# Kernel optimization log

Hardware: AMD Instinct MI355X
Metric: run time of the kernel (lower is better)

Reference implementation:

```python
import jax, jax.numpy as jnp
import numpy as np

DIN = 256
N_RATIOS = 3          # cfg.ANCHOR_RATIOS = [0.5, 1, 2]
NC_SCORE = N_RATIOS * 2   # 6
NC_BBOX = N_RATIOS * 4    # 12
LEVEL_SHAPES = [(150, 250), (75, 125), (38, 63), (19, 32), (10, 16)]


def setup_inputs() -> dict:
    key = jax.random.key(0)
    ks = jax.random.split(key, 12)
    inp = {}
    for i, (h, w) in enumerate(LEVEL_SHAPES):
        inp[f"rpn_feat_p{i+2}"] = jax.random.normal(ks[i], (4, DIN, h, w), dtype=jnp.float32)
    inp["im_info"] = jnp.ones((4, 3), dtype=jnp.float32)
    s = 0.01
    inp["W_conv"] = jax.random.normal(ks[5], (512, DIN, 3, 3), dtype=jnp.float32) * s
    inp["b_conv"] = jnp.zeros((512,), dtype=jnp.float32)
    inp["W_cls"] = jax.random.normal(ks[6], (NC_SCORE, 512), dtype=jnp.float32) * s
    inp["b_cls"] = jnp.zeros((NC_SCORE,), dtype=jnp.float32)
    inp["W_box"] = jax.random.normal(ks[7], (NC_BBOX, 512), dtype=jnp.float32) * s
    inp["b_box"] = jnp.zeros((NC_BBOX,), dtype=jnp.float32)
    return inp


def _conv3x3(x, W, b):
    y = jax.lax.conv_general_dilated(
        x, W, window_strides=(1, 1), padding="SAME",
        dimension_numbers=("NCHW", "OIHW", "NCHW"))
    return y + b[None, :, None, None]


def _level_head(feat, W_conv, b_conv, W_cls, b_cls, W_box, b_box):
    B = feat.shape[0]
    conv1 = jax.nn.relu(_conv3x3(feat, W_conv, b_conv))            # [B,512,H,W]
    score = jnp.einsum("bchw,oc->bohw", conv1, W_cls) + b_cls[None, :, None, None]  # [B,6,H,W]
    bbox = jnp.einsum("bchw,oc->bohw", conv1, W_box) + b_box[None, :, None, None]   # [B,12,H,W]
    _, C, H, W = score.shape
    # reshape(x, 2): view(B, 2, C*H/2, W), softmax over dim 1, reshape back
    prob = jax.nn.softmax(score.reshape(B, 2, (C * H) // 2, W), axis=1).reshape(B, C, H, W)
    score_f = score.transpose(0, 2, 3, 1).reshape(B, -1, 2)
    prob_f = prob.transpose(0, 2, 3, 1).reshape(B, -1, 2)
    bbox_f = bbox.transpose(0, 2, 3, 1).reshape(B, -1, 4)
    return score_f, prob_f, bbox_f


def reference(rpn_feat_p2, rpn_feat_p3, rpn_feat_p4, rpn_feat_p5, rpn_feat_p6,
              im_info, W_conv, b_conv, W_cls, b_cls, W_box, b_box):
    feats = [rpn_feat_p2, rpn_feat_p3, rpn_feat_p4, rpn_feat_p5, rpn_feat_p6]
    scores, probs, boxes = [], [], []
    for f in feats:  # fixed 5 FPN levels
        s, p, b = _level_head(f, W_conv, b_conv, W_cls, b_cls, W_box, b_box)
        scores.append(s); probs.append(p); boxes.append(b)
    rpn_cls_score_alls = jnp.concatenate(scores, axis=1)            # [B, N, 2]
    rpn_cls_prob_alls = jnp.concatenate(probs, axis=1)              # [B, N, 2]
    rpn_bbox_pred_alls = jnp.concatenate(boxes, axis=1)             # [B, N, 4]
    return rpn_cls_score_alls, rpn_cls_prob_alls, rpn_bbox_pred_alls
```

## Files before the change

### kernel.cpp

```cpp
#include <hip/hip_runtime.h>
#include <stdint.h>


typedef __bf16 bf16x8 __attribute__((ext_vector_type(8)));
typedef float  f32x4  __attribute__((ext_vector_type(4)));

#define WS_WR2_OFF   0
#define WS_WH2_OFF   2359296
#define WS_SB_OFF    2392064
#define WS_FP_OFF    17100800
#define WS_TOTAL     123197440

__device__ __forceinline__ unsigned short f2bf(float f) {
    unsigned u = __builtin_bit_cast(unsigned, f);
    unsigned r = (u + 0x7FFF + ((u >> 16) & 1)) >> 16;
    return (unsigned short)r;
}

__device__ __forceinline__ void gl_lds16(const void* g, void* l) {
    __builtin_amdgcn_global_load_lds(
        (const __attribute__((address_space(1))) unsigned int*)g,
        (__attribute__((address_space(3))) unsigned int*)l, 16, 0, 0);
}

__global__ __launch_bounds__(256) void prep_weights(
    const float* __restrict__ Wc, const float* __restrict__ Wcls,
    const float* __restrict__ Wbox,
    unsigned short* __restrict__ wr2, unsigned short* __restrict__ wh2)
{
    int idx = blockIdx.x * 256 + threadIdx.x;
    if (idx < 1179648) {
        int o = idx / 2304;
        int k = idx - o * 2304;
        int r = k >> 8, c = k & 255;
        wr2[idx] = f2bf(Wc[o * 2304 + c * 9 + r]);
    } else {
        int i2 = idx - 1179648;
        if (i2 < 9216) {
            int j = i2 >> 9, o = i2 & 511;
            float v = (j < 6) ? Wcls[j * 512 + o] : Wbox[(j - 6) * 512 + o];
            wh2[j * 512 + o] = f2bf(v);
        }
    }
}

__global__ __launch_bounds__(256) void prep_feats(
    const float* __restrict__ f0, const float* __restrict__ f1,
    const float* __restrict__ f2, const float* __restrict__ f3,
    const float* __restrict__ f4, unsigned short* __restrict__ fpad)
{
    __shared__ unsigned short lds[64 * 258];
    int bi = blockIdx.x;
    int b = bi / 817;
    int r = bi - b * 817;
    const float* fsrc; int H, W, Wp, h, wb; long lb;
    if (r < 600)      { fsrc=f0; H=150; W=250; Wp=252; h=r>>2; wb=r&3; lb=32768    + (long)b*9805824; }
    else if (r < 750) { int rr=r-600; fsrc=f1; H=75; W=125; Wp=127; h=rr>>1; wb=rr&1; lb=39288832 + (long)b*2503424; }
    else if (r < 788) { fsrc=f2; H=38; W=63; Wp=65; h=r-750; wb=0; lb=49335296 + (long)b*665600; }
    else if (r < 807) { fsrc=f3; H=19; W=32; Wp=34; h=r-788; wb=0; lb=52030464 + (long)b*182784; }
    else              { fsrc=f4; H=10; W=16; Wp=18; h=r-807; wb=0; lb=52794368 + (long)b*55296; }
    const int t = threadIdx.x;
    const long cstr = (long)H * W;
    const int w = t & 63;
    const int wg = wb * 64 + w;
    const bool wv = (wg < W);
    const float* src = fsrc + (((long)b * 256) * H + h) * W + wg;
    unsigned* ldsw = (unsigned*)lds;
    #pragma unroll 4
    for (int it = 0; it < 32; ++it) {
        int c0 = (t >> 6) * 2 + it * 8;
        float v0 = wv ? src[(long)c0 * cstr] : 0.0f;
        float v1 = wv ? src[(long)(c0 + 1) * cstr] : 0.0f;
        unsigned pk = (unsigned)f2bf(v0) | ((unsigned)f2bf(v1) << 16);
        ldsw[w * 129 + (c0 >> 1)] = pk;
    }
    __syncthreads();
    #pragma unroll
    for (int k = 0; k < 8; ++k) {
        int g  = k * 256 + t;
        int px = g >> 5;
        int pg = wb * 64 + px;
        if (pg >= W) continue;
        int d0 = px * 129 + (g & 31) * 4;
        uint4 v;
        v.x = ldsw[d0]; v.y = ldsw[d0 + 1]; v.z = ldsw[d0 + 2]; v.w = ldsw[d0 + 3];
        unsigned short* dst = fpad + lb + (long)((h + 1) * Wp + (pg + 1)) * 256 + (g & 31) * 8;
        *(uint4*)dst = v;
    }
}

__global__ __launch_bounds__(256) void conv_main(
    const unsigned short* __restrict__ fpad,
    const unsigned short* __restrict__ wr2,
    const unsigned short* __restrict__ wh2,
    const float* __restrict__ b_conv,
    float* __restrict__ sbuf)
{
    __shared__ unsigned short smem[16384];
    const int tid = threadIdx.x;
    const int bx = blockIdx.x;
    const int tile = bx >> 2, chunk = bx & 3;
    int b = tile / 399;
    int tr = tile - b * 399;
    int Wp, lt; long lb;
    if (tr < 296)      { lt = tr;       Wp = 252; lb = 32768    + (long)b * 9805824; }
    else if (tr < 371) { lt = tr - 296; Wp = 127; lb = 39288832 + (long)b * 2503424; }
    else if (tr < 391) { lt = tr - 371; Wp = 65;  lb = 49335296 + (long)b * 665600;  }
    else if (tr < 397) { lt = tr - 391; Wp = 34;  lb = 52030464 + (long)b * 182784;  }
    else               { lt = tr - 397; Wp = 18;  lb = 52794368 + (long)b * 55296;   }

    const int arow  = tid >> 3;
    const int aslot = (tid & 7) ^ (arow & 7);
    const long apix = lb + (long)(Wp + lt * 128 + arow) * 256 + aslot * 8;
    const long bofs = (long)(chunk * 128 + arow) * 2304 + aslot * 8;

    const int wv = tid >> 6, lane = tid & 63;
    char* lA = (char*)smem + wv * 1024;
    char* lB = (char*)smem + 16384 + wv * 1024;
    const int mrow = (wv & 1) * 64, ncol = (wv >> 1) * 64;
    const int mr = lane & 15;
    const int kq = (lane >> 4) * 8;
    const int m7 = mr & 7;

    f32x4 acc[4][4];
    #pragma unroll
    for (int mt = 0; mt < 4; ++mt)
        #pragma unroll
        for (int nt = 0; nt < 4; ++nt) acc[mt][nt] = (f32x4){0.f, 0.f, 0.f, 0.f};

    for (int r = 0; r < 9; ++r) {
        const int doff = (r / 3 - 1) * Wp + (r % 3 - 1);
        const unsigned short* ga = fpad + apix + (long)doff * 256;
        const unsigned short* gb = wr2 + bofs + r * 256;
        for (int cb = 0; cb < 4; ++cb) {
            const unsigned short* ga2 = ga + cb * 64;
            const unsigned short* gb2 = gb + cb * 64;
            #pragma unroll
            for (int i = 0; i < 4; ++i) {
                gl_lds16(ga2 + i * 8192,  lA + i * 4096);
                gl_lds16(gb2 + i * 73728, lB + i * 4096);
            }
            __syncthreads();
            #pragma unroll
            for (int kk = 0; kk < 64; kk += 32) {
                const int sx = ((((kk >> 3) + (lane >> 4)) ^ m7) << 3);
                bf16x8 af[4], bfr[4];
                #pragma unroll
                for (int mt = 0; mt < 4; ++mt)
                    af[mt] = *(const bf16x8*)&smem[(mrow + mt * 16 + mr) * 64 + sx];
                #pragma unroll
                for (int nt = 0; nt < 4; ++nt)
                    bfr[nt] = *(const bf16x8*)&smem[8192 + (ncol + nt * 16 + mr) * 64 + sx];
                #pragma unroll
                for (int mt = 0; mt < 4; ++mt)
                    #pragma unroll
                    for (int nt = 0; nt < 4; ++nt)
                        acc[mt][nt] = __builtin_amdgcn_mfma_f32_16x16x32_bf16(
                            af[mt], bfr[nt], acc[mt][nt], 0, 0, 0);
            }
            __syncthreads();
        }
    }

    float bias[4];
    #pragma unroll
    for (int nt = 0; nt < 4; ++nt) bias[nt] = b_conv[chunk * 128 + ncol + nt * 16 + mr];
    #pragma unroll
    for (int mt = 0; mt < 4; ++mt)
        #pragma unroll
        for (int nt = 0; nt < 4; ++nt)
            #pragma unroll
            for (int q = 0; q < 4; ++q) {
                int row = mrow + mt * 16 + (lane >> 4) * 4 + q;
                int col = ncol + nt * 16 + mr;
                int sl  = (col >> 3) ^ (row & 7);
                smem[row * 128 + (sl << 3) + (col & 7)] =
                    f2bf(fmaxf(acc[mt][nt][q] + bias[nt], 0.0f));
            }
    __syncthreads();

    f32x4 acc2[2][2];
    #pragma unroll
    for (int mi = 0; mi < 2; ++mi)
        #pragma unroll
        for (int ni = 0; ni < 2; ++ni) acc2[mi][ni] = (f32x4){0.f, 0.f, 0.f, 0.f};
    #pragma unroll
    for (int ks = 0; ks < 4; ++ks) {
        const int sg = ks * 4 + (lane >> 4);
        bf16x8 ha[2], hb[2];
        #pragma unroll
        for (int mi = 0; mi < 2; ++mi) {
            int rowH = (wv * 2 + mi) * 16 + mr;
            ha[mi] = *(const bf16x8*)&smem[rowH * 128 + ((sg ^ m7) << 3)];
        }
        #pragma unroll
        for (int ni = 0; ni < 2; ++ni)
            hb[ni] = *(const bf16x8*)&wh2[(ni * 16 + mr) * 512 + chunk * 128 + ks * 32 + kq];
        #pragma unroll
        for (int mi = 0; mi < 2; ++mi)
            #pragma unroll
            for (int ni = 0; ni < 2; ++ni)
                acc2[mi][ni] = __builtin_amdgcn_mfma_f32_16x16x32_bf16(
                    ha[mi], hb[ni], acc2[mi][ni], 0, 0, 0);
    }
    const long slotbase = (long)tile * 128;
    #pragma unroll
    for (int ni = 0; ni < 2; ++ni) {
        int j = ni * 16 + mr;
        if (j < 18) {
            #pragma unroll
            for (int mi = 0; mi < 2; ++mi)
                #pragma unroll
                for (int q = 0; q < 4; ++q) {
                    int row = (wv * 2 + mi) * 16 + (lane >> 4) * 4 + q;
                    atomicAdd(&sbuf[(slotbase + row) * 18 + j], acc2[mi][ni][q]);
                }
        }
    }
}

__global__ __launch_bounds__(256) void finalize(
    const float* __restrict__ sbuf, const float* __restrict__ b_cls,
    const float* __restrict__ b_box, float* __restrict__ out)
{
    int idx = blockIdx.x * 256 + threadIdx.x;
    int tile = idx >> 7, m = idx & 127;
    int b = tile / 399;
    int tr = tile - b * 399;
    int hp, wp, H, W, noff;
    if (tr < 296)      { int f = 252 + (tr)       * 128 + m; hp = f / 252; wp = f - hp * 252; H = 150; W = 250; noff = 0; }
    else if (tr < 371) { int f = 127 + (tr - 296) * 128 + m; hp = f / 127; wp = f - hp * 127; H = 75;  W = 125; noff = 112500; }
    else if (tr < 391) { int f = 65  + (tr - 371) * 128 + m; hp = f / 65;  wp = f - hp * 65;  H = 38;  W = 63;  noff = 140625; }
    else if (tr < 397) { int f = 34  + (tr - 391) * 128 + m; hp = f / 34;  wp = f - hp * 34;  H = 19;  W = 32;  noff = 147807; }
    else               { int f = 18  + (tr - 397) * 128 + m; hp = f / 18;  wp = f - hp * 18;  H = 10;  W = 16;  noff = 149631; }
    if (hp < 1 || hp > H || wp < 1 || wp > W) return;

    const float* s = sbuf + (long)idx * 18;
    float sc[6], bb[12], pr[6];
    #pragma unroll
    for (int c = 0; c < 6; ++c) sc[c] = s[c] + b_cls[c];
    #pragma unroll
    for (int k = 0; k < 12; ++k) bb[k] = s[6 + k] + b_box[k];
    #pragma unroll
    for (int c = 0; c < 6; ++c) {
        int p = (c < 3) ? c + 3 : c - 3;
        pr[c] = 1.0f / (1.0f + expf(sc[p] - sc[c]));
    }
    int n = noff + ((hp - 1) * W + (wp - 1)) * 3;
    long o0 = ((long)b * 150111 + n) * 2;
    float* O0 = out + o0;
    float* O1 = out + 1200888 + o0;
    float* O2 = out + 2401776 + ((long)b * 150111 + n) * 4;
    #pragma unroll
    for (int c = 0; c < 6; ++c) { O0[c] = sc[c]; O1[c] = pr[c]; }
    #pragma unroll
    for (int k = 0; k < 12; ++k) O2[k] = bb[k];
}

extern "C" void kernel_launch(void* const* d_in, const int* in_sizes, int n_in,
                              void* d_out, int out_size, void* d_ws, size_t ws_size,
                              hipStream_t stream)
{
    const float* f0   = (const float*)d_in[0];
    const float* f1   = (const float*)d_in[1];
    const float* f2   = (const float*)d_in[2];
    const float* f3   = (const float*)d_in[3];
    const float* f4   = (const float*)d_in[4];
    const float* Wc   = (const float*)d_in[6];
    const float* bC   = (const float*)d_in[7];
    const float* Wcls = (const float*)d_in[8];
    const float* bcls = (const float*)d_in[9];
    const float* Wbox = (const float*)d_in[10];
    const float* bbox = (const float*)d_in[11];

    unsigned short* wr2  = (unsigned short*)((char*)d_ws + WS_WR2_OFF);
    unsigned short* wh2  = (unsigned short*)((char*)d_ws + WS_WH2_OFF);
    float*          sbuf = (float*)((char*)d_ws + WS_SB_OFF);
    unsigned short* fpad = (unsigned short*)((char*)d_ws + WS_FP_OFF);

    hipMemsetAsync(d_ws, 0, (size_t)WS_TOTAL, stream);
    hipLaunchKernelGGL(prep_weights, dim3(4644), dim3(256), 0, stream, Wc, Wcls, Wbox, wr2, wh2);
    hipLaunchKernelGGL(prep_feats,   dim3(3268), dim3(256), 0, stream, f0, f1, f2, f3, f4, fpad);
    hipLaunchKernelGGL(conv_main,    dim3(6384), dim3(256), 0, stream, fpad, wr2, wh2, bC, sbuf);
    hipLaunchKernelGGL(finalize,     dim3(798),  dim3(256), 0, stream, sbuf, bcls, bbox, (float*)d_out);
}
```

Before: 892.2 us.

## Zero only padding rings instead of whole workspace, and remap conv block order

Replaces the full-workspace memset (about 123MB) with a memset of only the score buffer, plus a small kernel that zeroes just the halo border pixels of the padded bf16 feature maps. It also zero-pads the head weight buffer to 32 rows, since that region is no longer cleared. conv_main blocks are remapped so that 8 spatial tiles share each weight chunk consecutively, which is meant to improve L2 reuse of weights; the grid is padded with an early-exit guard. The risk is correctness: any padded region that is neither written by prep_feats nor zeroed by the ring kernel would now hold stale data.

```diff
diff --git a/kernel.cpp b/kernel.cpp
--- a/kernel.cpp
+++ b/kernel.cpp
@@ -36,12 +36,37 @@
         wr2[idx] = f2bf(Wc[o * 2304 + c * 9 + r]);
     } else {
         int i2 = idx - 1179648;
-        if (i2 < 9216) {
+        if (i2 < 16384) {
             int j = i2 >> 9, o = i2 & 511;
-            float v = (j < 6) ? Wcls[j * 512 + o] : Wbox[(j - 6) * 512 + o];
+            float v = (j < 6) ? Wcls[j * 512 + o]
+                    : (j < 18) ? Wbox[(j - 6) * 512 + o] : 0.0f;
             wh2[j * 512 + o] = f2bf(v);
         }
     }
+}
+
+__global__ __launch_bounds__(256) void zero_rings(unsigned short* __restrict__ fpad)
+{
+    int idx = blockIdx.x * 256 + threadIdx.x;
+    int b = idx / 50432;
+    int rem = idx - b * 50432;
+    int Wp, H, W; long lb;
+    if (rem < 25728)      {               Wp=252; H=150; W=250; lb=32768    + (long)b*9805824; }
+    else if (rem < 38656) { rem -= 25728; Wp=127; H=75;  W=125; lb=39288832 + (long)b*2503424; }
+    else if (rem < 45248) { rem -= 38656; Wp=65;  H=38;  W=63;  lb=49335296 + (long)b*665600;  }
+    else if (rem < 48640) { rem -= 45248; Wp=34;  H=19;  W=32;  lb=52030464 + (long)b*182784;  }
+    else                  { rem -= 48640; Wp=18;  H=10;  W=16;  lb=52794368 + (long)b*55296;   }
+    int c = rem >> 5, slot = rem & 31;
+    int h, w;
+    if (c < Wp)          { h = 0;     w = c; }
+    else if (c < 2 * Wp) { h = H + 1; w = c - Wp; }
+    else {
+        int c2 = c - 2 * Wp;
+        h = 1 + (c2 >> 1);
+        w = (c2 & 1) ? (W + 1) : 0;
+    }
+    uint4 z = {0u, 0u, 0u, 0u};
+    *(uint4*)(fpad + lb + (long)(h * Wp + w) * 256 + slot * 8) = z;
 }
 
 __global__ __launch_bounds__(256) void prep_feats(
@@ -98,8 +123,10 @@
 {
     __shared__ unsigned short smem[16384];
     const int tid = threadIdx.x;
-    const int bx = blockIdx.x;
-    const int tile = bx >> 2, chunk = bx & 3;
+    const int bid = blockIdx.x;
+    const int tile = ((bid >> 5) << 3) + (bid & 7);
+    const int chunk = (bid >> 3) & 3;
+    if (tile >= 1596) return;
     int b = tile / 399;
     int tr = tile - b * 399;
     int Wp, lt; long lb;
@@ -278,9 +305,10 @@
     float*          sbuf = (float*)((char*)d_ws + WS_SB_OFF);
     unsigned short* fpad = (unsigned short*)((char*)d_ws + WS_FP_OFF);
 
-    hipMemsetAsync(d_ws, 0, (size_t)WS_TOTAL, stream);
-    hipLaunchKernelGGL(prep_weights, dim3(4644), dim3(256), 0, stream, Wc, Wcls, Wbox, wr2, wh2);
+    hipMemsetAsync((char*)d_ws + WS_SB_OFF, 0, (size_t)(WS_FP_OFF - WS_SB_OFF), stream);
+    hipLaunchKernelGGL(prep_weights, dim3(4672), dim3(256), 0, stream, Wc, Wcls, Wbox, wr2, wh2);
+    hipLaunchKernelGGL(zero_rings,   dim3(788),  dim3(256), 0, stream, fpad);
     hipLaunchKernelGGL(prep_feats,   dim3(3268), dim3(256), 0, stream, f0, f1, f2, f3, f4, fpad);
-    hipLaunchKernelGGL(conv_main,    dim3(6384), dim3(256), 0, stream, fpad, wr2, wh2, bC, sbuf);
+    hipLaunchKernelGGL(conv_main,    dim3(6400), dim3(256), 0, stream, fpad, wr2, wh2, bC, sbuf);
     hipLaunchKernelGGL(finalize,     dim3(798),  dim3(256), 0, stream, sbuf, bcls, bbox, (float*)d_out);
 }
```

New measurement: 886.1 us. No clear change (-0.7%).
